# Performance work log

Measured on AMD Instinct MI355X. Metric: run time of the kernel, lower is better.

The kernel has to match this reference:

```python
import jax, jax.numpy as jnp
import numpy as np

N_NODES = 100000
N_EDGES = 1600000
IN_DIM, HID_DIM, OUT_DIM = 512, 128, 64
BN_EPS = 1e-5


def setup_inputs() -> dict:
    key = jax.random.key(0)
    ks = jax.random.split(key, 8)
    x = jax.random.normal(ks[0], (N_NODES, IN_DIM), dtype=jnp.float32)
    edge_index = jax.random.randint(ks[1], (2, N_EDGES), 0, N_NODES, dtype=jnp.int64)
    W1 = jax.random.normal(ks[2], (IN_DIM, HID_DIM), dtype=jnp.float32) / np.sqrt(IN_DIM)
    b1 = jnp.zeros((HID_DIM,), dtype=jnp.float32)
    W2 = jax.random.normal(ks[3], (HID_DIM, OUT_DIM), dtype=jnp.float32) / np.sqrt(HID_DIM)
    b2 = jnp.zeros((OUT_DIM,), dtype=jnp.float32)
    gamma = jnp.ones((HID_DIM,), dtype=jnp.float32)
    beta = jnp.zeros((HID_DIM,), dtype=jnp.float32)
    return {"x": x, "edge_index": edge_index, "W1": W1, "b1": b1,
            "W2": W2, "b2": b2, "gamma": gamma, "beta": beta}


def _gcn_conv(x, src, dst, W, b):
    # PyG GCNConv(normalize=False): transform then sum-aggregate src->dst, no self-loops
    h = x @ W                                   # [N, out]
    agg = jax.ops.segment_sum(h[src], dst, num_segments=N_NODES)
    return agg + b


def _batchnorm(h, gamma, beta):
    mean = jnp.mean(h, axis=0)
    var = jnp.mean(jnp.square(h - mean), axis=0)  # biased var (training mode)
    return (h - mean) * jax.lax.rsqrt(var + BN_EPS) * gamma + beta


def reference(x, edge_index, W1, b1, W2, b2, gamma, beta):
    src, dst = edge_index[0], edge_index[1]
    h = _gcn_conv(x, src, dst, W1, b1)          # [N, HID]
    h = _batchnorm(h, gamma, beta)
    h = jax.nn.relu(h)
    h = _gcn_conv(h, src, dst, W2, b2)          # [N, OUT]
    # F.normalize(p=2, dim=1), eps=1e-12
    norm = jnp.linalg.norm(h, axis=1, keepdims=True)
    return h / jnp.maximum(norm, 1e-12)
```

## Files before the change

kernel.cpp:

```cpp
#include <hip/hip_runtime.h>
#include <hip/hip_bf16.h>
#include <stdint.h>

#define NN 100000
#define NE 1600000
#define IND 512
#define HID 128
#define OUTD 64
#define BN_EPS 1e-5f
#define NP 98
#define PSZ 1024
#define PCAP 20480
#define BINCH 8192
#define NBIN 196

typedef __attribute__((ext_vector_type(8))) short short8v;
typedef __attribute__((ext_vector_type(4))) float f32x4;

__device__ __forceinline__ ushort f2bf(float f, float& back) {
  uint u = __float_as_uint(f);
  uint r = u + 0x7FFFu + ((u >> 16) & 1u);
  ushort h = (ushort)(r >> 16);
  back = __uint_as_float(((uint)h) << 16);
  return h;
}
__device__ __forceinline__ ushort f2bf_n(float f) {
  uint u = __float_as_uint(f);
  uint r = u + 0x7FFFu + ((u >> 16) & 1u);
  return (ushort)(r >> 16);
}
__device__ __forceinline__ float bf2f(ushort h) {
  return __uint_as_float(((uint)h) << 16);
}
__device__ __forceinline__ float bflo(uint v) { return __uint_as_float(v << 16); }
__device__ __forceinline__ float bfhi(uint v) { return __uint_as_float(v & 0xffff0000u); }
__device__ __forceinline__ uint packbf(float lo, float hi) {
  return (uint)f2bf_n(lo) | ((uint)f2bf_n(hi) << 16);
}

__device__ __forceinline__ int edge_at(const int* e32, int f, int i) {
  if (f) return (int)((const long long*)e32)[i];
  return e32[i];
}

__global__ __launch_bounds__(256) void k_prep(const int* __restrict__ edges,
                                              const float* __restrict__ W1,
                                              const float* __restrict__ W2,
                                              int* __restrict__ flag,
                                              ushort* __restrict__ Wth,
                                              ushort* __restrict__ Wtl,
                                              ushort* __restrict__ W2th,
                                              ushort* __restrict__ W2tl) {
  const int bid = blockIdx.x, tid = threadIdx.x;
  if (bid == 0) {
    __shared__ int nz;
    if (tid == 0) nz = 0;
    __syncthreads();
    if (tid < 64) {
      int v = edges[2 * tid + 1];
      if (v != 0) atomicAdd(&nz, 1);
    }
    __syncthreads();
    if (tid == 0) *flag = (nz == 0) ? 1 : 0;
    return;
  }
  if (bid <= 256) {
    int i = (bid - 1) * 256 + tid;
    int n = i >> 9, k = i & 511;
    float w = W1[(size_t)k * HID + n];
    float back;
    Wth[i] = f2bf(w, back);
    Wtl[i] = f2bf_n(w - back);
    return;
  }
  {
    int j = (bid - 257) * 256 + tid;
    int n = j >> 7, k = j & 127;
    float w = W2[(size_t)k * OUTD + n];
    float back;
    W2th[j] = f2bf(w, back);
    W2tl[j] = f2bf_n(w - back);
  }
}

__device__ void bin_body(int bid, ushort* smem16, const int* edges,
                         const int* flag, int* gCursor, int* staging) {
  int* cnt   = (int*)smem16;
  int* scn   = cnt + 128;
  int* base  = cnt + 256;
  int* cur   = cnt + 384;
  int* items = cnt + 512;
  const int tid = threadIdx.x;
  const int e0 = bid * BINCH;
  const int ecnt = min(BINCH, NE - e0);
  const int f = *flag;
  for (int i = tid; i < NP; i += 256) cnt[i] = 0;
  __syncthreads();
  for (int i = tid; i < ecnt; i += 256) {
    int d = edge_at(edges, f, NE + e0 + i);
    atomicAdd(&cnt[d >> 10], 1);
  }
  __syncthreads();
  if (tid == 0) {
    int s = 0;
    for (int p = 0; p < NP; ++p) { scn[p] = s; s += cnt[p]; }
  }
  __syncthreads();
  if (tid < NP) {
    base[tid] = (cnt[tid] > 0) ? atomicAdd(&gCursor[tid], cnt[tid]) : 0;
    cur[tid] = 0;
  }
  __syncthreads();
  for (int i = tid; i < ecnt; i += 256) {
    int d = edge_at(edges, f, NE + e0 + i);
    int s = edge_at(edges, f, e0 + i);
    int p = d >> 10;
    int lp = atomicAdd(&cur[p], 1);
    items[scn[p] + lp] = (s << 10) | (d & (PSZ - 1));
  }
  __syncthreads();
  for (int p = 0; p < NP; ++p) {
    int c = cnt[p];
    if (c == 0) continue;
    int gb = base[p];
    int* dst = staging + (size_t)p * PCAP;
    for (int i = tid; i < c; i += 256) {
      int gpos = gb + i;
      if (gpos < PCAP) dst[gpos] = items[scn[p] + i];
    }
  }
}

__device__ void gemm1_body(int bid, ushort* smem, const float* x,
                           const ushort* Wth, const ushort* Wtl,
                           ushort* h1b) {
  ushort* sOut = smem;
  const int tid = threadIdx.x;
  const int lane = tid & 63, wid = tid >> 6;
  const int wr = wid >> 1, wc = wid & 1;
  const int lrow = lane & 15, lkg = lane >> 4;
  const int row0 = bid * 128;

  f32x4 acc[4][4];
#pragma unroll
  for (int m = 0; m < 4; ++m)
#pragma unroll
    for (int n = 0; n < 4; ++n) acc[m][n] = (f32x4){0.f, 0.f, 0.f, 0.f};

  float4 ra[4];
  uint4 rbh[2], rbl[2];

#pragma unroll
  for (int i = 0; i < 4; ++i) {
    int flat = i * 256 + tid, r = flat >> 3, kq = flat & 7;
    int grow = row0 + r; if (grow > NN - 1) grow = NN - 1;
    ra[i] = *(const float4*)(x + (size_t)grow * IND + kq * 4);
  }
#pragma unroll
  for (int i = 0; i < 2; ++i) {
    int flat = i * 256 + tid, col = flat >> 2, kc = flat & 3;
    rbh[i] = *(const uint4*)(Wth + (size_t)col * IND + kc * 8);
    rbl[i] = *(const uint4*)(Wtl + (size_t)col * IND + kc * 8);
  }
  {
    ushort* dAh = smem;
    ushort* dBh = smem + 5120;
    ushort* dBl = smem + 10240;
#pragma unroll
    for (int i = 0; i < 4; ++i) {
      int flat = i * 256 + tid, r = flat >> 3, kq = flat & 7;
      ushort4 hi;
      hi.x = f2bf_n(ra[i].x); hi.y = f2bf_n(ra[i].y);
      hi.z = f2bf_n(ra[i].z); hi.w = f2bf_n(ra[i].w);
      *(ushort4*)&dAh[r * 40 + kq * 4] = hi;
    }
#pragma unroll
    for (int i = 0; i < 2; ++i) {
      int flat = i * 256 + tid, col = flat >> 2, kc = flat & 3;
      *(uint4*)&dBh[col * 40 + kc * 8] = rbh[i];
      *(uint4*)&dBl[col * 40 + kc * 8] = rbl[i];
    }
  }

  int cur = 0;
  for (int s = 0; s < 16; ++s) {
    __syncthreads();
    if (s < 15) {
      int kt = (s + 1) * 32;
#pragma unroll
      for (int i = 0; i < 4; ++i) {
        int flat = i * 256 + tid, r = flat >> 3, kq = flat & 7;
        int grow = row0 + r; if (grow > NN - 1) grow = NN - 1;
        ra[i] = *(const float4*)(x + (size_t)grow * IND + kt + kq * 4);
      }
#pragma unroll
      for (int i = 0; i < 2; ++i) {
        int flat = i * 256 + tid, col = flat >> 2, kc = flat & 3;
        rbh[i] = *(const uint4*)(Wth + (size_t)col * IND + kt + kc * 8);
        rbl[i] = *(const uint4*)(Wtl + (size_t)col * IND + kt + kc * 8);
      }
    }
    {
      const ushort* bAh = smem + cur * 15360;
      const ushort* bBh = bAh + 5120;
      const ushort* bBl = bAh + 10240;
      short8v ah[4], bh[4], bl[4];
#pragma unroll
      for (int m = 0; m < 4; ++m) {
        int r = wr * 64 + m * 16 + lrow;
        ah[m] = *(const short8v*)&bAh[r * 40 + lkg * 8];
      }
#pragma unroll
      for (int n = 0; n < 4; ++n) {
        int c = wc * 64 + n * 16 + lrow;
        bh[n] = *(const short8v*)&bBh[c * 40 + lkg * 8];
        bl[n] = *(const short8v*)&bBl[c * 40 + lkg * 8];
      }
#pragma unroll
      for (int m = 0; m < 4; ++m)
#pragma unroll
        for (int n = 0; n < 4; ++n) {
          acc[m][n] = __builtin_amdgcn_mfma_f32_16x16x32_bf16(ah[m], bh[n], acc[m][n], 0, 0, 0);
          acc[m][n] = __builtin_amdgcn_mfma_f32_16x16x32_bf16(ah[m], bl[n], acc[m][n], 0, 0, 0);
        }
    }
    if (s < 15) {
      ushort* dAh = smem + (cur ^ 1) * 15360;
      ushort* dBh = dAh + 5120;
      ushort* dBl = dAh + 10240;
#pragma unroll
      for (int i = 0; i < 4; ++i) {
        int flat = i * 256 + tid, r = flat >> 3, kq = flat & 7;
        ushort4 hi;
        hi.x = f2bf_n(ra[i].x); hi.y = f2bf_n(ra[i].y);
        hi.z = f2bf_n(ra[i].z); hi.w = f2bf_n(ra[i].w);
        *(ushort4*)&dAh[r * 40 + kq * 4] = hi;
      }
#pragma unroll
      for (int i = 0; i < 2; ++i) {
        int flat = i * 256 + tid, col = flat >> 2, kc = flat & 3;
        *(uint4*)&dBh[col * 40 + kc * 8] = rbh[i];
        *(uint4*)&dBl[col * 40 + kc * 8] = rbl[i];
      }
    }
    cur ^= 1;
  }

  __syncthreads();
#pragma unroll
  for (int m = 0; m < 4; ++m)
#pragma unroll
    for (int i = 0; i < 4; ++i) {
      int lr = wr * 64 + m * 16 + lkg * 4 + i;
#pragma unroll
      for (int n = 0; n < 4; ++n)
        sOut[lr * 136 + wc * 64 + n * 16 + lrow] = f2bf_n(acc[m][n][i]);
    }
  __syncthreads();
#pragma unroll
  for (int j = 0; j < 8; ++j) {
    int flat = j * 256 + tid;
    int r = flat >> 4, c = flat & 15;
    int grow = row0 + r;
    if (grow < NN)
      *(uint4*)(h1b + (size_t)grow * HID + c * 8) =
          *(const uint4*)&sOut[r * 136 + c * 8];
  }
}

__global__ __launch_bounds__(256) void k_fused1(const float* __restrict__ x,
                                                const ushort* __restrict__ Wth,
                                                const ushort* __restrict__ Wtl,
                                                const int* __restrict__ edges,
                                                const int* __restrict__ flag,
                                                int* __restrict__ gCursor,
                                                int* __restrict__ staging,
                                                ushort* __restrict__ h1b) {
  __shared__ __align__(16) ushort smem[30720];
  if (blockIdx.x < NBIN)
    bin_body(blockIdx.x, smem, edges, flag, gCursor, staging);
  else
    gemm1_body(blockIdx.x - NBIN, smem, x, Wth, Wtl, h1b);
}

__global__ __launch_bounds__(256) void k_csrpart(const int* __restrict__ staging,
                                                 const int* __restrict__ gCursor,
                                                 int* __restrict__ offsets,
                                                 int* __restrict__ csr_src) {
  __shared__ int cnt[PSZ];
  __shared__ int cur[PSZ];
  __shared__ int tsum[256];
  __shared__ int srcbuf[PCAP];
  __shared__ int gbase_s;
  const int tid = threadIdx.x;
  const int p = blockIdx.x;
  if (tid == 0) {
    int s = 0;
    for (int q = 0; q < p; ++q) s += min(gCursor[q], PCAP);
    gbase_s = s;
    if (p == NP - 1) offsets[NN] = NE;
  }
  const int tot = min(gCursor[p], PCAP);
  const int* st = staging + (size_t)p * PCAP;
  for (int i = tid; i < PSZ; i += 256) { cnt[i] = 0; cur[i] = 0; }
  __syncthreads();
  const int gbase = gbase_s;
  for (int i = tid; i < tot; i += 256) atomicAdd(&cnt[st[i] & (PSZ - 1)], 1);
  __syncthreads();
  int b0 = tid * 4;
  int c0 = cnt[b0], c1 = cnt[b0 + 1], c2 = cnt[b0 + 2], c3 = cnt[b0 + 3];
  int ls = c0 + c1 + c2 + c3;
  tsum[tid] = ls;
  __syncthreads();
  for (int off = 1; off < 256; off <<= 1) {
    int t = (tid >= off) ? tsum[tid - off] : 0;
    __syncthreads();
    tsum[tid] += t;
    __syncthreads();
  }
  int ebase = tsum[tid] - ls;
  cnt[b0] = ebase;
  cnt[b0 + 1] = ebase + c0;
  cnt[b0 + 2] = ebase + c0 + c1;
  cnt[b0 + 3] = ebase + c0 + c1 + c2;
  __syncthreads();
  for (int i = tid; i < PSZ; i += 256) {
    int node = p * PSZ + i;
    if (node < NN) offsets[node] = gbase + cnt[i];
  }
  for (int i = tid; i < tot; i += 256) {
    int item = st[i];
    int dl = item & (PSZ - 1);
    int lp = atomicAdd(&cur[dl], 1);
    srcbuf[cnt[dl] + lp] = item >> 10;
  }
  __syncthreads();
  for (int i = tid; i < tot; i += 256) csr_src[gbase + i] = srcbuf[i];
}

__global__ __launch_bounds__(256) void k_agg1(const ushort* __restrict__ h1b,
                                              const int* __restrict__ offsets,
                                              const int* __restrict__ csr_src,
                                              const float* __restrict__ b1,
                                              ushort* __restrict__ aggb) {
  int w = threadIdx.x >> 6, lane = threadIdx.x & 63;
  int n = blockIdx.x * 4 + w;
  if (n >= NN) return;
  int beg = offsets[n], end = offsets[n + 1];
  int half = lane >> 5, ch = lane & 31;
  const uint2* h = (const uint2*)h1b;
  float4 a = {0.f, 0.f, 0.f, 0.f}, a2 = {0.f, 0.f, 0.f, 0.f};
  int i = beg + half;
  for (; i + 2 < end; i += 4) {
    uint2 v0 = h[(size_t)csr_src[i] * 32 + ch];
    uint2 v1 = h[(size_t)csr_src[i + 2] * 32 + ch];
    a.x += bflo(v0.x); a.y += bfhi(v0.x); a.z += bflo(v0.y); a.w += bfhi(v0.y);
    a2.x += bflo(v1.x); a2.y += bfhi(v1.x); a2.z += bflo(v1.y); a2.w += bfhi(v1.y);
  }
  if (i < end) {
    uint2 v = h[(size_t)csr_src[i] * 32 + ch];
    a.x += bflo(v.x); a.y += bfhi(v.x); a.z += bflo(v.y); a.w += bfhi(v.y);
  }
  a.x += a2.x; a.y += a2.y; a.z += a2.z; a.w += a2.w;
  a.x += __shfl_xor(a.x, 32);
  a.y += __shfl_xor(a.y, 32);
  a.z += __shfl_xor(a.z, 32);
  a.w += __shfl_xor(a.w, 32);
  if (half == 0) {
    float4 b = *(const float4*)(b1 + 4 * ch);
    uint2 o;
    o.x = packbf(a.x + b.x, a.y + b.y);
    o.y = packbf(a.z + b.z, a.w + b.w);
    ((uint2*)aggb)[(size_t)n * 32 + ch] = o;
  }
}

__global__ __launch_bounds__(256) void k_bnstats(const ushort* __restrict__ aggb,
                                                 float* __restrict__ gsum,
                                                 float* __restrict__ gsq) {
  __shared__ float2 ss[4][64], qq[4][64];
  int tid = threadIdx.x;
  int lane = tid & 63, g = tid >> 6;
  int r0 = blockIdx.x * 128;
  const uint* a = (const uint*)aggb;
  float2 s = {0.f, 0.f}, q = {0.f, 0.f};
  for (int k = 0; k < 32; ++k) {
    int r = r0 + g + 4 * k;
    if (r < NN) {
      uint v = a[(size_t)r * 64 + lane];
      float lo = bflo(v), hi = bfhi(v);
      s.x += lo; s.y += hi;
      q.x += lo * lo; q.y += hi * hi;
    }
  }
  ss[g][lane] = s; qq[g][lane] = q;
  __syncthreads();
  if (g == 0) {
    float2 S = ss[0][lane], Q = qq[0][lane];
#pragma unroll
    for (int gg = 1; gg < 4; ++gg) {
      S.x += ss[gg][lane].x; S.y += ss[gg][lane].y;
      Q.x += qq[gg][lane].x; Q.y += qq[gg][lane].y;
    }
    atomicAdd(&gsum[2 * lane], S.x);
    atomicAdd(&gsum[2 * lane + 1], S.y);
    atomicAdd(&gsq[2 * lane], Q.x);
    atomicAdd(&gsq[2 * lane + 1], Q.y);
  }
}

__global__ __launch_bounds__(256) void k_gemm2m(const ushort* __restrict__ aggb,
                                                const ushort* __restrict__ W2th,
                                                const ushort* __restrict__ W2tl,
                                                const float* __restrict__ gsum,
                                                const float* __restrict__ gsq,
                                                const float* __restrict__ gamma,
                                                const float* __restrict__ beta,
                                                ushort* __restrict__ h2b) {
  __shared__ __align__(16) ushort smem[27648];
  __shared__ float isgS[128], bbS[128];
  ushort* sBh = smem;
  ushort* sBl = smem + 8704;
  ushort* sA  = smem + 17408;
  ushort* sOut = sA;
  const int tid = threadIdx.x;
  const int lane = tid & 63, wid = tid >> 6;
  const int wr = wid >> 1, wc = wid & 1;
  const int lrow = lane & 15, lkg = lane >> 4;
  const int row0 = blockIdx.x * 128;

  if (tid < 128) {
    float mean = gsum[tid] * (1.f / NN);
    float var = fmaxf(gsq[tid] * (1.f / NN) - mean * mean, 0.f);
    float inv = 1.f / sqrtf(var + BN_EPS);
    float g = gamma[tid] * inv;
    isgS[tid] = g;
    bbS[tid] = beta[tid] - mean * g;
  }
#pragma unroll
  for (int i = 0; i < 4; ++i) {
    int c = i * 256 + tid;
    int n = c >> 4, kq = c & 15;
    *(uint4*)&sBh[n * 136 + kq * 8] = *(const uint4*)(W2th + (size_t)n * HID + kq * 8);
    *(uint4*)&sBl[n * 136 + kq * 8] = *(const uint4*)(W2tl + (size_t)n * HID + kq * 8);
  }

  f32x4 acc[4][2];
#pragma unroll
  for (int m = 0; m < 4; ++m)
#pragma unroll
    for (int n = 0; n < 2; ++n) acc[m][n] = (f32x4){0.f, 0.f, 0.f, 0.f};

  uint4 rA[2];
#pragma unroll
  for (int i = 0; i < 2; ++i) {
    int c = i * 256 + tid;
    int r = c >> 2, cq = c & 3;
    int grow = row0 + r; if (grow > NN - 1) grow = NN - 1;
    rA[i] = *(const uint4*)(aggb + (size_t)grow * HID + cq * 8);
  }
  __syncthreads();

  {
    ushort* dA = sA;
#pragma unroll
    for (int i = 0; i < 2; ++i) {
      int c = i * 256 + tid;
      int r = c >> 2, cq = c & 3;
      int k0 = cq * 8;
      uint4 v = rA[i];
      uint o[4];
      const uint* vv = (const uint*)&v;
#pragma unroll
      for (int j = 0; j < 4; ++j) {
        float lo = bflo(vv[j]), hi = bfhi(vv[j]);
        lo = fmaxf(fmaf(lo, isgS[k0 + 2 * j], bbS[k0 + 2 * j]), 0.f);
        hi = fmaxf(fmaf(hi, isgS[k0 + 2 * j + 1], bbS[k0 + 2 * j + 1]), 0.f);
        o[j] = packbf(lo, hi);
      }
      *(uint4*)&dA[r * 40 + cq * 8] = *(const uint4*)o;
    }
  }

  int cur = 0;
  for (int s = 0; s < 4; ++s) {
    __syncthreads();
    const int kt = s * 32;
    if (s < 3) {
      int ktn = kt + 32;
#pragma unroll
      for (int i = 0; i < 2; ++i) {
        int c = i * 256 + tid;
        int r = c >> 2, cq = c & 3;
        int grow = row0 + r; if (grow > NN - 1) grow = NN - 1;
        rA[i] = *(const uint4*)(aggb + (size_t)grow * HID + ktn + cq * 8);
      }
    }
    {
      const ushort* bA = sA + cur * 5120;
      short8v ah[4], bh[2], bl[2];
#pragma unroll
      for (int m = 0; m < 4; ++m) {
        int r = wr * 64 + m * 16 + lrow;
        ah[m] = *(const short8v*)&bA[r * 40 + lkg * 8];
      }
#pragma unroll
      for (int n = 0; n < 2; ++n) {
        int c = wc * 32 + n * 16 + lrow;
        bh[n] = *(const short8v*)&sBh[c * 136 + kt + lkg * 8];
        bl[n] = *(const short8v*)&sBl[c * 136 + kt + lkg * 8];
      }
#pragma unroll
      for (int m = 0; m < 4; ++m)
#pragma unroll
        for (int n = 0; n < 2; ++n) {
          acc[m][n] = __builtin_amdgcn_mfma_f32_16x16x32_bf16(ah[m], bh[n], acc[m][n], 0, 0, 0);
          acc[m][n] = __builtin_amdgcn_mfma_f32_16x16x32_bf16(ah[m], bl[n], acc[m][n], 0, 0, 0);
        }
    }
    if (s < 3) {
      ushort* dA = sA + (cur ^ 1) * 5120;
      int k0b = (s + 1) * 32;
#pragma unroll
      for (int i = 0; i < 2; ++i) {
        int c = i * 256 + tid;
        int r = c >> 2, cq = c & 3;
        int k0 = k0b + cq * 8;
        uint4 v = rA[i];
        uint o[4];
        const uint* vv = (const uint*)&v;
#pragma unroll
        for (int j = 0; j < 4; ++j) {
          float lo = bflo(vv[j]), hi = bfhi(vv[j]);
          lo = fmaxf(fmaf(lo, isgS[k0 + 2 * j], bbS[k0 + 2 * j]), 0.f);
          hi = fmaxf(fmaf(hi, isgS[k0 + 2 * j + 1], bbS[k0 + 2 * j + 1]), 0.f);
          o[j] = packbf(lo, hi);
        }
        *(uint4*)&dA[r * 40 + cq * 8] = *(const uint4*)o;
      }
    }
    cur ^= 1;
  }

  __syncthreads();
#pragma unroll
  for (int m = 0; m < 4; ++m)
#pragma unroll
    for (int i = 0; i < 4; ++i) {
      int lr = wr * 64 + m * 16 + lkg * 4 + i;
#pragma unroll
      for (int n = 0; n < 2; ++n)
        sOut[lr * 72 + wc * 32 + n * 16 + lrow] = f2bf_n(acc[m][n][i]);
    }
  __syncthreads();
#pragma unroll
  for (int i = 0; i < 4; ++i) {
    int c = i * 256 + tid;
    int r = c >> 3, cq = c & 7;
    int grow = row0 + r;
    if (grow < NN)
      *(uint4*)(h2b + (size_t)grow * OUTD + cq * 8) =
          *(const uint4*)&sOut[r * 72 + cq * 8];
  }
}

__global__ __launch_bounds__(256) void k_agg2norm(const ushort* __restrict__ h2b,
                                                  const int* __restrict__ offsets,
                                                  const int* __restrict__ csr_src,
                                                  const float* __restrict__ b2,
                                                  float* __restrict__ out) {
  int w = threadIdx.x >> 6, lane = threadIdx.x & 63;
  int n = blockIdx.x * 4 + w;
  if (n >= NN) return;
  int beg = offsets[n], end = offsets[n + 1];
  int half = lane >> 5, ch = lane & 31;
  const uint* h = (const uint*)h2b;
  float2 a = {0.f, 0.f}, a2 = {0.f, 0.f};
  int i = beg + half;
  for (; i + 2 < end; i += 4) {
    uint v0 = h[(size_t)csr_src[i] * 32 + ch];
    uint v1 = h[(size_t)csr_src[i + 2] * 32 + ch];
    a.x += bflo(v0); a.y += bfhi(v0);
    a2.x += bflo(v1); a2.y += bfhi(v1);
  }
  if (i < end) {
    uint v = h[(size_t)csr_src[i] * 32 + ch];
    a.x += bflo(v); a.y += bfhi(v);
  }
  a.x += a2.x; a.y += a2.y;
  a.x += __shfl_xor(a.x, 32);
  a.y += __shfl_xor(a.y, 32);
  float2 b = *(const float2*)(b2 + 2 * ch);
  a.x += b.x; a.y += b.y;
  float q = a.x * a.x + a.y * a.y;
#pragma unroll
  for (int off = 16; off > 0; off >>= 1) q += __shfl_xor(q, off);
  float norm = sqrtf(q);
  float scale = 1.f / fmaxf(norm, 1e-12f);
  if (half == 0) {
    float2 o = {a.x * scale, a.y * scale};
    *(float2*)(out + (size_t)n * OUTD + 2 * ch) = o;
  }
}

extern "C" void kernel_launch(void* const* d_in, const int* in_sizes, int n_in,
                              void* d_out, int out_size, void* d_ws, size_t ws_size,
                              hipStream_t stream) {
  const float* x     = (const float*)d_in[0];
  const int*   edges = (const int*)d_in[1];
  const float* W1    = (const float*)d_in[2];
  const float* b1    = (const float*)d_in[3];
  const float* W2    = (const float*)d_in[4];
  const float* b2    = (const float*)d_in[5];
  const float* gamma = (const float*)d_in[6];
  const float* beta  = (const float*)d_in[7];

  char* ws = (char*)d_ws;
  ushort* h1b     = (ushort*)(ws);
  ushort* aggb    = (ushort*)(ws + 26000000);
  int*    csr_src = (int*)(ws + 77500000);
  int*    offsets = (int*)(ws + 84000000);
  int*    staging = (int*)(ws + 84400128);
  int*    gCursor = (int*)(ws + 92428544);
  int*    partBase= (int*)(ws + 92429056);
  float*  gsum    = (float*)(ws + 92429568);
  float*  gsq     = (float*)(ws + 92430080);
  int*    eflag   = (int*)(ws + 92431616);
  ushort* Wth     = (ushort*)(ws + 92432128);
  ushort* Wtl     = (ushort*)(ws + 92563200);
  ushort* W2th    = (ushort*)(ws + 92694272);
  ushort* W2tl    = (ushort*)(ws + 92710656);
  ushort* h2b     = h1b;
  (void)partBase;

  if (ws_size < 92727040) return;

  hipMemsetAsync(gCursor, 0, 2048, stream);

  k_prep<<<289, 256, 0, stream>>>(edges, W1, W2, eflag, Wth, Wtl, W2th, W2tl);
  k_fused1<<<NBIN + 782, 256, 0, stream>>>(x, Wth, Wtl, edges, eflag,
                                           gCursor, staging, h1b);
  k_csrpart<<<NP, 256, 0, stream>>>(staging, gCursor, offsets, csr_src);
  k_agg1<<<25000, 256, 0, stream>>>(h1b, offsets, csr_src, b1, aggb);
  k_bnstats<<<782, 256, 0, stream>>>(aggb, gsum, gsq);
  k_gemm2m<<<782, 256, 0, stream>>>(aggb, W2th, W2tl, gsum, gsq, gamma, beta, h2b);
  k_agg2norm<<<25000, 256, 0, stream>>>(h2b, offsets, csr_src, b2,
                                        (float*)d_out);
}
```

Baseline: 309.5 us.

## Fuse BN statistics into agg1, halve CSR partition size, stage neighbor indices in LDS

Partitioning now uses 196 partitions of 512 nodes, which doubles the number of k_csrpart blocks and parallelises the per-partition prefix offsets with a block scan. k_agg1 becomes a grid-stride kernel that also accumulates the BatchNorm sum and sum-of-squares through LDS atomics followed by global atomics, so the separate k_bnstats pass over aggb goes away. Both aggregation kernels copy up to 64 neighbor indices per node into LDS with one coalesced load before gathering. The trade-offs are LDS atomic contention in agg1, fewer resident blocks, and a slightly different floating-point summation order.

```diff
diff --git a/kernel.cpp b/kernel.cpp
--- a/kernel.cpp
+++ b/kernel.cpp
@@ -8,11 +8,12 @@
 #define HID 128
 #define OUTD 64
 #define BN_EPS 1e-5f
-#define NP 98
-#define PSZ 1024
-#define PCAP 20480
+#define NP 196
+#define PSZ 512
+#define PCAP 10240
 #define BINCH 8192
 #define NBIN 196
+#define AGG1_GRID 2048
 
 typedef __attribute__((ext_vector_type(8))) short short8v;
 typedef __attribute__((ext_vector_type(4))) float f32x4;
@@ -86,10 +87,10 @@
 __device__ void bin_body(int bid, ushort* smem16, const int* edges,
                          const int* flag, int* gCursor, int* staging) {
   int* cnt   = (int*)smem16;
-  int* scn   = cnt + 128;
-  int* base  = cnt + 256;
-  int* cur   = cnt + 384;
-  int* items = cnt + 512;
+  int* scn   = cnt + NP;
+  int* base  = cnt + 2 * NP;
+  int* cur   = cnt + 3 * NP;
+  int* items = cnt + 4 * NP;
   const int tid = threadIdx.x;
   const int e0 = bid * BINCH;
   const int ecnt = min(BINCH, NE - e0);
@@ -98,7 +99,7 @@
   __syncthreads();
   for (int i = tid; i < ecnt; i += 256) {
     int d = edge_at(edges, f, NE + e0 + i);
-    atomicAdd(&cnt[d >> 10], 1);
+    atomicAdd(&cnt[d >> 9], 1);
   }
   __syncthreads();
   if (tid == 0) {
@@ -114,7 +115,7 @@
   for (int i = tid; i < ecnt; i += 256) {
     int d = edge_at(edges, f, NE + e0 + i);
     int s = edge_at(edges, f, e0 + i);
-    int p = d >> 10;
+    int p = d >> 9;
     int lp = atomicAdd(&cur[p], 1);
     items[scn[p] + lp] = (s << 10) | (d & (PSZ - 1));
   }
@@ -290,26 +291,28 @@
   __shared__ int cnt[PSZ];
   __shared__ int cur[PSZ];
   __shared__ int tsum[256];
+  __shared__ int gc[256];
   __shared__ int srcbuf[PCAP];
-  __shared__ int gbase_s;
   const int tid = threadIdx.x;
   const int p = blockIdx.x;
-  if (tid == 0) {
-    int s = 0;
-    for (int q = 0; q < p; ++q) s += min(gCursor[q], PCAP);
-    gbase_s = s;
-    if (p == NP - 1) offsets[NN] = NE;
+  gc[tid] = (tid < NP) ? min(gCursor[tid], PCAP) : 0;
+  for (int i = tid; i < PSZ; i += 256) { cnt[i] = 0; cur[i] = 0; }
+  if (p == NP - 1 && tid == 0) offsets[NN] = NE;
+  __syncthreads();
+  for (int off = 1; off < 256; off <<= 1) {
+    int t = (tid >= off) ? gc[tid - off] : 0;
+    __syncthreads();
+    gc[tid] += t;
+    __syncthreads();
   }
   const int tot = min(gCursor[p], PCAP);
+  const int gbase = gc[p] - tot;
   const int* st = staging + (size_t)p * PCAP;
-  for (int i = tid; i < PSZ; i += 256) { cnt[i] = 0; cur[i] = 0; }
-  __syncthreads();
-  const int gbase = gbase_s;
   for (int i = tid; i < tot; i += 256) atomicAdd(&cnt[st[i] & (PSZ - 1)], 1);
   __syncthreads();
-  int b0 = tid * 4;
-  int c0 = cnt[b0], c1 = cnt[b0 + 1], c2 = cnt[b0 + 2], c3 = cnt[b0 + 3];
-  int ls = c0 + c1 + c2 + c3;
+  int b0 = tid * 2;
+  int c0 = cnt[b0], c1 = cnt[b0 + 1];
+  int ls = c0 + c1;
   tsum[tid] = ls;
   __syncthreads();
   for (int off = 1; off < 256; off <<= 1) {
@@ -321,8 +324,6 @@
   int ebase = tsum[tid] - ls;
   cnt[b0] = ebase;
   cnt[b0 + 1] = ebase + c0;
-  cnt[b0 + 2] = ebase + c0 + c1;
-  cnt[b0 + 3] = ebase + c0 + c1 + c2;
   __syncthreads();
   for (int i = tid; i < PSZ; i += 256) {
     int node = p * PSZ + i;
@@ -342,70 +343,59 @@
                                               const int* __restrict__ offsets,
                                               const int* __restrict__ csr_src,
                                               const float* __restrict__ b1,
-                                              ushort* __restrict__ aggb) {
-  int w = threadIdx.x >> 6, lane = threadIdx.x & 63;
-  int n = blockIdx.x * 4 + w;
-  if (n >= NN) return;
-  int beg = offsets[n], end = offsets[n + 1];
-  int half = lane >> 5, ch = lane & 31;
+                                              ushort* __restrict__ aggb,
+                                              float* __restrict__ gsum,
+                                              float* __restrict__ gsq) {
+  __shared__ float sSum[128], sSq[128];
+  __shared__ int sidx[4][64];
+  const int tid = threadIdx.x, w = tid >> 6, lane = tid & 63;
+  const int half = lane >> 5, ch = lane & 31;
+  for (int i = tid; i < 128; i += 256) { sSum[i] = 0.f; sSq[i] = 0.f; }
+  __syncthreads();
   const uint2* h = (const uint2*)h1b;
-  float4 a = {0.f, 0.f, 0.f, 0.f}, a2 = {0.f, 0.f, 0.f, 0.f};
-  int i = beg + half;
-  for (; i + 2 < end; i += 4) {
-    uint2 v0 = h[(size_t)csr_src[i] * 32 + ch];
-    uint2 v1 = h[(size_t)csr_src[i + 2] * 32 + ch];
-    a.x += bflo(v0.x); a.y += bfhi(v0.x); a.z += bflo(v0.y); a.w += bfhi(v0.y);
-    a2.x += bflo(v1.x); a2.y += bfhi(v1.x); a2.z += bflo(v1.y); a2.w += bfhi(v1.y);
-  }
-  if (i < end) {
-    uint2 v = h[(size_t)csr_src[i] * 32 + ch];
-    a.x += bflo(v.x); a.y += bfhi(v.x); a.z += bflo(v.y); a.w += bfhi(v.y);
-  }
-  a.x += a2.x; a.y += a2.y; a.z += a2.z; a.w += a2.w;
-  a.x += __shfl_xor(a.x, 32);
-  a.y += __shfl_xor(a.y, 32);
-  a.z += __shfl_xor(a.z, 32);
-  a.w += __shfl_xor(a.w, 32);
-  if (half == 0) {
-    float4 b = *(const float4*)(b1 + 4 * ch);
-    uint2 o;
-    o.x = packbf(a.x + b.x, a.y + b.y);
-    o.y = packbf(a.z + b.z, a.w + b.w);
-    ((uint2*)aggb)[(size_t)n * 32 + ch] = o;
-  }
-}
-
-__global__ __launch_bounds__(256) void k_bnstats(const ushort* __restrict__ aggb,
-                                                 float* __restrict__ gsum,
-                                                 float* __restrict__ gsq) {
-  __shared__ float2 ss[4][64], qq[4][64];
-  int tid = threadIdx.x;
-  int lane = tid & 63, g = tid >> 6;
-  int r0 = blockIdx.x * 128;
-  const uint* a = (const uint*)aggb;
-  float2 s = {0.f, 0.f}, q = {0.f, 0.f};
-  for (int k = 0; k < 32; ++k) {
-    int r = r0 + g + 4 * k;
-    if (r < NN) {
-      uint v = a[(size_t)r * 64 + lane];
-      float lo = bflo(v), hi = bfhi(v);
-      s.x += lo; s.y += hi;
-      q.x += lo * lo; q.y += hi * hi;
-    }
-  }
-  ss[g][lane] = s; qq[g][lane] = q;
-  __syncthreads();
-  if (g == 0) {
-    float2 S = ss[0][lane], Q = qq[0][lane];
-#pragma unroll
-    for (int gg = 1; gg < 4; ++gg) {
-      S.x += ss[gg][lane].x; S.y += ss[gg][lane].y;
-      Q.x += qq[gg][lane].x; Q.y += qq[gg][lane].y;
-    }
-    atomicAdd(&gsum[2 * lane], S.x);
-    atomicAdd(&gsum[2 * lane + 1], S.y);
-    atomicAdd(&gsq[2 * lane], Q.x);
-    atomicAdd(&gsq[2 * lane + 1], Q.y);
+  float4 b = *(const float4*)(b1 + 4 * ch);
+  for (int n = blockIdx.x * 4 + w; n < NN; n += AGG1_GRID * 4) {
+    int beg = offsets[n], end = offsets[n + 1], deg = end - beg;
+    int dcap = min(deg, 64);
+    if (lane < dcap) sidx[w][lane] = csr_src[beg + lane];
+    float4 a = {0.f, 0.f, 0.f, 0.f}, a2 = {0.f, 0.f, 0.f, 0.f};
+    int i = half;
+    for (; i + 2 < dcap; i += 4) {
+      int s0 = sidx[w][i], s1 = sidx[w][i + 2];
+      uint2 v0 = h[(size_t)s0 * 32 + ch];
+      uint2 v1 = h[(size_t)s1 * 32 + ch];
+      a.x += bflo(v0.x); a.y += bfhi(v0.x); a.z += bflo(v0.y); a.w += bfhi(v0.y);
+      a2.x += bflo(v1.x); a2.y += bfhi(v1.x); a2.z += bflo(v1.y); a2.w += bfhi(v1.y);
+    }
+    if (i < dcap) {
+      uint2 v = h[(size_t)sidx[w][i] * 32 + ch];
+      a.x += bflo(v.x); a.y += bfhi(v.x); a.z += bflo(v.y); a.w += bfhi(v.y);
+    }
+    for (int j = 64 + half; j < deg; j += 2) {
+      uint2 v = h[(size_t)csr_src[beg + j] * 32 + ch];
+      a.x += bflo(v.x); a.y += bfhi(v.x); a.z += bflo(v.y); a.w += bfhi(v.y);
+    }
+    a.x += a2.x; a.y += a2.y; a.z += a2.z; a.w += a2.w;
+    a.x += __shfl_xor(a.x, 32);
+    a.y += __shfl_xor(a.y, 32);
+    a.z += __shfl_xor(a.z, 32);
+    a.w += __shfl_xor(a.w, 32);
+    if (half == 0) {
+      float c0 = a.x + b.x, c1 = a.y + b.y, c2 = a.z + b.z, c3 = a.w + b.w;
+      uint2 o;
+      o.x = packbf(c0, c1);
+      o.y = packbf(c2, c3);
+      ((uint2*)aggb)[(size_t)n * 32 + ch] = o;
+      atomicAdd(&sSum[4 * ch + 0], c0); atomicAdd(&sSq[4 * ch + 0], c0 * c0);
+      atomicAdd(&sSum[4 * ch + 1], c1); atomicAdd(&sSq[4 * ch + 1], c1 * c1);
+      atomicAdd(&sSum[4 * ch + 2], c2); atomicAdd(&sSq[4 * ch + 2], c2 * c2);
+      atomicAdd(&sSum[4 * ch + 3], c3); atomicAdd(&sSq[4 * ch + 3], c3 * c3);
+    }
+  }
+  __syncthreads();
+  if (tid < 128) {
+    atomicAdd(&gsum[tid], sSum[tid]);
+    atomicAdd(&gsq[tid], sSq[tid]);
   }
 }
 
@@ -569,22 +559,29 @@
                                                   const int* __restrict__ csr_src,
                                                   const float* __restrict__ b2,
                                                   float* __restrict__ out) {
-  int w = threadIdx.x >> 6, lane = threadIdx.x & 63;
+  __shared__ int sidx[4][64];
+  int tid = threadIdx.x, w = tid >> 6, lane = tid & 63;
   int n = blockIdx.x * 4 + w;
   if (n >= NN) return;
-  int beg = offsets[n], end = offsets[n + 1];
+  int beg = offsets[n], end = offsets[n + 1], deg = end - beg;
+  int dcap = min(deg, 64);
+  if (lane < dcap) sidx[w][lane] = csr_src[beg + lane];
   int half = lane >> 5, ch = lane & 31;
   const uint* h = (const uint*)h2b;
   float2 a = {0.f, 0.f}, a2 = {0.f, 0.f};
-  int i = beg + half;
-  for (; i + 2 < end; i += 4) {
-    uint v0 = h[(size_t)csr_src[i] * 32 + ch];
-    uint v1 = h[(size_t)csr_src[i + 2] * 32 + ch];
+  int i = half;
+  for (; i + 2 < dcap; i += 4) {
+    uint v0 = h[(size_t)sidx[w][i] * 32 + ch];
+    uint v1 = h[(size_t)sidx[w][i + 2] * 32 + ch];
     a.x += bflo(v0); a.y += bfhi(v0);
     a2.x += bflo(v1); a2.y += bfhi(v1);
   }
-  if (i < end) {
-    uint v = h[(size_t)csr_src[i] * 32 + ch];
+  if (i < dcap) {
+    uint v = h[(size_t)sidx[w][i] * 32 + ch];
+    a.x += bflo(v); a.y += bfhi(v);
+  }
+  for (int j = 64 + half; j < deg; j += 2) {
+    uint v = h[(size_t)csr_src[beg + j] * 32 + ch];
     a.x += bflo(v); a.y += bfhi(v);
   }
   a.x += a2.x; a.y += a2.y;
@@ -622,7 +619,6 @@
   int*    offsets = (int*)(ws + 84000000);
   int*    staging = (int*)(ws + 84400128);
   int*    gCursor = (int*)(ws + 92428544);
-  int*    partBase= (int*)(ws + 92429056);
   float*  gsum    = (float*)(ws + 92429568);
   float*  gsq     = (float*)(ws + 92430080);
   int*    eflag   = (int*)(ws + 92431616);
@@ -631,7 +627,6 @@
   ushort* W2th    = (ushort*)(ws + 92694272);
   ushort* W2tl    = (ushort*)(ws + 92710656);
   ushort* h2b     = h1b;
-  (void)partBase;
 
   if (ws_size < 92727040) return;
 
@@ -641,8 +636,7 @@
   k_fused1<<<NBIN + 782, 256, 0, stream>>>(x, Wth, Wtl, edges, eflag,
                                            gCursor, staging, h1b);
   k_csrpart<<<NP, 256, 0, stream>>>(staging, gCursor, offsets, csr_src);
-  k_agg1<<<25000, 256, 0, stream>>>(h1b, offsets, csr_src, b1, aggb);
-  k_bnstats<<<782, 256, 0, stream>>>(aggb, gsum, gsq);
+  k_agg1<<<AGG1_GRID, 256, 0, stream>>>(h1b, offsets, csr_src, b1, aggb, gsum, gsq);
   k_gemm2m<<<782, 256, 0, stream>>>(aggb, W2th, W2tl, gsum, gsq, gamma, beta, h2b);
   k_agg2norm<<<25000, 256, 0, stream>>>(h2b, offsets, csr_src, b2,
                                         (float*)d_out);
```

New measurement: 334.9 us. +8.2%, slower.
